# Kernel tuning notes

Hardware: AMD Instinct MI355X
Metric: run time of the kernel (lower is better)

The kernel has to match this reference:

```python
import jax, jax.numpy as jnp
import numpy as np

MG = (5, 5)          # mesh_grid_size
UP = (17, 17)        # upsample_size
IMG = (512.0, 512.0) # image_size
B = 8192
FC_OUT = MG[0] * MG[1] * 2  # 50
KH = (UP[0] - 1) // (MG[0] - 1) + 1  # 5
KW = (UP[1] - 1) // (MG[1] - 1) + 1  # 5
SH = (UP[0] - 1) // (MG[0] - 1)      # 4
SW = (UP[1] - 1) // (MG[1] - 1)      # 4
L0 = MG[0] - 1
L1 = MG[1] - 1


def _grid(h, w):
    # channel 0: x coords vary along rows (image_size[0]); channel 1: y along cols
    x_t = jnp.broadcast_to(jnp.linspace(0.0, IMG[0], h)[:, None], (h, w))
    y_t = jnp.broadcast_to(jnp.linspace(0.0, IMG[1], w)[None, :], (h, w))
    return jnp.stack([x_t, y_t], 0)  # [2, h, w]


def _unfold22(a):
    # a: [B, 2, H, W] -> [B, (H-1)*(W-1), 4, 2]; 4 = kernel positions row-major, 2 = channel
    p = jnp.stack([a[:, :, :-1, :-1], a[:, :, :-1, 1:],
                   a[:, :, 1:, :-1], a[:, :, 1:, 1:]], axis=2)  # [B,2,4,H-1,W-1]
    return p.reshape(a.shape[0], 2, 4, -1).transpose(0, 3, 2, 1)


def _persp(src, dst):
    # exact 4-point homography solve (torchgeometry.get_perspective_transform)
    x0, y0 = src[..., 0], src[..., 1]
    u, v = dst[..., 0], dst[..., 1]
    z = jnp.zeros_like(x0)
    o = jnp.ones_like(x0)
    ax = jnp.stack([x0, y0, o, z, z, z, -u * x0, -u * y0], -1)  # [N,4,8]
    ay = jnp.stack([z, z, z, x0, y0, o, -v * x0, -v * y0], -1)
    A = jnp.concatenate([ax, ay], 1)                 # [N,8,8]
    bb = jnp.concatenate([u, v], 1)[..., None]       # [N,8,1]
    h = jnp.linalg.solve(A, bb)[..., 0]              # [N,8]
    return jnp.concatenate([h, o[:, :1]], 1).reshape(-1, 3, 3)


def setup_inputs() -> dict:
    key = jax.random.key(0)
    ks = jax.random.split(key, 4)
    def lin(k, i, o):
        return jax.random.normal(k, (i, o), jnp.float32) / jnp.sqrt(i)
    return {
        "x": jax.random.normal(ks[0], (B, 1024), jnp.float32),
        "W1": lin(ks[1], 1024, 1024), "b1": jnp.zeros((1024,), jnp.float32),
        "W2": lin(ks[2], 1024, 2048), "b2": jnp.zeros((2048,), jnp.float32),
        "W3": lin(ks[3], 2048, FC_OUT), "b3": jnp.zeros((FC_OUT,), jnp.float32),
    }


def reference(x, W1, b1, W2, b2, W3, b3):
    Bn = x.shape[0]
    h = jax.nn.relu(x @ W1 + b1)
    h = jax.nn.relu(h @ W2 + b2)
    out = (h @ W3 + b3).reshape(Bn, 2, MG[0], MG[1])  # [B,2,5,5] mesh flow

    # sparse control grid and 2x2 patch corner points
    gs = _grid(MG[0], MG[1])
    src = _unfold22(jnp.broadcast_to(gs[None], (Bn, 2, MG[0], MG[1]))).reshape(-1, 4, 2)
    flow = _unfold22(out).reshape(-1, 4, 2)
    M = _persp(src, src + flow)  # [B*16, 3, 3]

    # dense grid and its unfold2 (kernel KHxKW, stride SHxSW) patch points
    gd = _grid(UP[0], UP[1])  # [2, 17, 17]
    gi = (np.arange(L0) * SH)[:, None, None, None] + np.arange(KH)[None, None, :, None]
    gj = (np.arange(L1) * SW)[None, :, None, None] + np.arange(KW)[None, None, None, :]
    I, J = np.broadcast_arrays(gi, gj)  # [L0,L1,KH,KW]
    pts = gd[:, I, J].transpose(1, 2, 3, 4, 0).reshape(1, L0 * L1, KH * KW, 2)
    pts = jnp.broadcast_to(pts, (Bn, L0 * L1, KH * KW, 2)).reshape(Bn * L0 * L1, KH * KW, 2)

    # transform_points: homogeneous warp + perspective divide
    ph = jnp.concatenate([pts, jnp.ones(pts.shape[:-1] + (1,), pts.dtype)], -1)
    oh = jnp.einsum('nij,npj->npi', M, ph)
    warped = oh[..., :2] / oh[..., 2:3]
    warped = warped.reshape(Bn, L0, L1, KH, KW, 2)

    # Fold: scatter-accumulate overlapping patches
    fold = jnp.zeros((Bn, 2, UP[0], UP[1]), x.dtype)
    for i in range(L0):
        for j in range(L1):
            blk = warped[:, i, j].transpose(0, 3, 1, 2)  # [B,2,KH,KW]
            fold = fold.at[:, :, i * SH:i * SH + KH, j * SW:j * SW + KW].add(blk)

    # boundary rescaling exactly as the torch code: only the 5x5 crossing points
    idx = np.arange(0, UP[0], MG[0] - 1)
    X, Y = np.meshgrid(idx, idx, indexing='xy')
    fold = fold.at[:, :, X, Y].multiply(0.5)
    for (a, b) in ((0, 0), (0, UP[1] - 1), (UP[0] - 1, UP[1] - 1), (UP[0] - 1, 0)):
        fold = fold.at[:, :, a, b].multiply(2.0)

    return fold - gd[None]  # upsampled mesh flow [B,2,17,17]
```

## Files before the change

kernel.cpp:

```cpp
#include <hip/hip_runtime.h>

typedef __bf16 bf16x8 __attribute__((ext_vector_type(8)));
typedef float f32x4 __attribute__((ext_vector_type(4)));

__device__ __forceinline__ unsigned short f2bf(float f) {
  unsigned int u = __builtin_bit_cast(unsigned int, f);
  unsigned int r = (u + 0x7fffu + ((u >> 16) & 1u)) >> 16;
  return (unsigned short)r;
}

__device__ __forceinline__ float bf2f(unsigned short u) {
  unsigned int v = ((unsigned int)u) << 16;
  return __builtin_bit_cast(float, v);
}

__device__ __forceinline__ void load16_lds(const unsigned short* g, unsigned short* l) {
  __builtin_amdgcn_global_load_lds(
      (const __attribute__((address_space(1))) void*)g,
      (__attribute__((address_space(3))) void*)l, 16, 0, 0);
}

__device__ __forceinline__ void wait_vm0() {
  asm volatile("s_waitcnt vmcnt(0)" ::: "memory");
  __builtin_amdgcn_sched_barrier(0);
}
__device__ __forceinline__ void barrier_raw() {
  __builtin_amdgcn_sched_barrier(0);
  __builtin_amdgcn_s_barrier();
  __builtin_amdgcn_sched_barrier(0);
}


__global__ __launch_bounds__(256) void prepass(
    const float* __restrict__ x, const float* __restrict__ W1,
    const float* __restrict__ W2, const float* __restrict__ W3,
    unsigned short* __restrict__ xbf, unsigned short* __restrict__ w1t,
    unsigned short* __restrict__ w2t, unsigned short* __restrict__ w3t) {
  __shared__ float tile[32][33];
  const int bid = blockIdx.x;
  const int t = threadIdx.x;
  if (bid < 2048) {
    for (int i = bid * 256 + t; i < 2097152; i += 2048 * 256) {
      float4 f = ((const float4*)x)[i];
      uint2 o;
      o.x = (unsigned)f2bf(f.x) | ((unsigned)f2bf(f.y) << 16);
      o.y = (unsigned)f2bf(f.z) | ((unsigned)f2bf(f.w) << 16);
      ((uint2*)xbf)[i] = o;
    }
  } else if (bid < 3072) {
    int ti = bid - 2048;
    int n0 = (ti & 31) * 32, k0 = (ti >> 5) * 32;
    int tx = t & 31, ty = t >> 5;
    #pragma unroll
    for (int r = 0; r < 32; r += 8)
      tile[ty + r][tx] = W1[(size_t)(k0 + ty + r) * 1024 + n0 + tx];
    __syncthreads();
    #pragma unroll
    for (int r = 0; r < 32; r += 8)
      w1t[(size_t)(n0 + ty + r) * 1024 + k0 + tx] = f2bf(tile[tx][ty + r]);
  } else if (bid < 5120) {
    int ti = bid - 3072;
    int n0 = (ti & 63) * 32, k0 = (ti >> 6) * 32;
    int tx = t & 31, ty = t >> 5;
    #pragma unroll
    for (int r = 0; r < 32; r += 8)
      tile[ty + r][tx] = W2[(size_t)(k0 + ty + r) * 2048 + n0 + tx];
    __syncthreads();
    #pragma unroll
    for (int r = 0; r < 32; r += 8)
      w2t[(size_t)(n0 + ty + r) * 1024 + k0 + tx] = f2bf(tile[tx][ty + r]);
  } else {
    int idx = (bid - 5120) * 256 + t;
    int n = idx >> 11, k = idx & 2047;
    w3t[idx] = f2bf((n < 50) ? W3[(size_t)k * 50 + n] : 0.f);
  }
}


__global__ __launch_bounds__(512, 4) void gemm1_v9(
    const unsigned short* __restrict__ A,
    const unsigned short* __restrict__ Bt,
    const float* __restrict__ bias,
    unsigned short* __restrict__ C) {
  constexpr int K = 1024, N = 1024, NT = 32;
  constexpr int AEL = 128 * 32;
  constexpr int BUF = 2 * AEL;
  __shared__ __align__(16) unsigned short smem[2 * BUF];
  const int t = threadIdx.x;
  const int m0 = blockIdx.x * 128;
  const int n0 = blockIdx.y * 128;
  const int lane = t & 63, wv = t >> 6;
  const int l16 = lane & 15, quad = lane >> 4;
  const int rb = (wv >> 1) * 32, cb = (wv & 1) * 64;

  const int tr = t >> 2;
  const int cg = ((t & 3) - (tr >> 1)) & 3;
  const unsigned short* Ag0 = A + (size_t)(m0 + tr) * K + cg * 8;
  const unsigned short* Bg0 = Bt + (size_t)(n0 + tr) * K + cg * 8;
  const int ldsO = wv * 512;

  f32x4 acc[2][4] = {};

  load16_lds(Ag0, &smem[ldsO]);
  load16_lds(Bg0, &smem[AEL + ldsO]);

  for (int kt = 0; kt < NT; ++kt) {
    unsigned short* Ls = &smem[(kt & 1) * BUF];

    wait_vm0();
    barrier_raw();

    if (kt + 1 < NT) {
      unsigned short* Ln = &smem[((kt + 1) & 1) * BUF];
      load16_lds(Ag0 + (size_t)(kt + 1) * 32, &Ln[ldsO]);
      load16_lds(Bg0 + (size_t)(kt + 1) * 32, &Ln[AEL + ldsO]);
    }

    bf16x8 af[2], bfr[4];
    #pragma unroll
    for (int ni = 0; ni < 4; ++ni) {
      int row = cb + ni * 16 + l16;
      bfr[ni] = *(const bf16x8*)&Ls[AEL + row * 32 + ((quad + (row >> 1)) & 3) * 8];
    }
    #pragma unroll
    for (int mi = 0; mi < 2; ++mi) {
      int row = rb + mi * 16 + l16;
      af[mi] = *(const bf16x8*)&Ls[row * 32 + ((quad + (row >> 1)) & 3) * 8];
    }
    #pragma unroll
    for (int mi = 0; mi < 2; ++mi)
      #pragma unroll
      for (int ni = 0; ni < 4; ++ni)
        acc[mi][ni] = __builtin_amdgcn_mfma_f32_16x16x32_bf16(
            af[mi], bfr[ni], acc[mi][ni], 0, 0, 0);
  }
  barrier_raw();

  unsigned short* Cs = smem;
  float bv[4];
  #pragma unroll
  for (int ni = 0; ni < 4; ++ni) bv[ni] = bias[n0 + cb + ni * 16 + l16];
  #pragma unroll
  for (int mi = 0; mi < 2; ++mi)
    #pragma unroll
    for (int ni = 0; ni < 4; ++ni)
      #pragma unroll
      for (int r = 0; r < 4; ++r) {
        int row = rb + mi * 16 + quad * 4 + r;
        int col = cb + ni * 16 + l16;
        int pb = (col >> 3) ^ (row & 15);
        Cs[row * 128 + pb * 8 + (col & 7)] = f2bf(fmaxf(acc[mi][ni][r] + bv[ni], 0.f));
      }
  __syncthreads();
  #pragma unroll
  for (int j = 0; j < 4; ++j) {
    int idx = j * 512 + t;
    int row = idx >> 4, cgc = idx & 15;
    int pb = cgc ^ (row & 15);
    *(uint4*)&C[(size_t)(m0 + row) * N + n0 + cgc * 8] =
        *(const uint4*)&Cs[row * 128 + pb * 8];
  }
}


__global__ __launch_bounds__(512, 4) void gemm2_v8(
    const unsigned short* __restrict__ A,
    const unsigned short* __restrict__ Bt,
    const float* __restrict__ bias,
    const unsigned short* __restrict__ W3t,
    unsigned short* __restrict__ part) {
  constexpr int K = 1024, NT = 32;
  constexpr int AEL = 256 * 32;
  constexpr int BEL = 128 * 32;
  constexpr int BUF = AEL + BEL;
  __shared__ __align__(16) unsigned short smem[32768];
  const int t = threadIdx.x;
  const int m0 = blockIdx.x * 256;
  const int n0 = blockIdx.y * 128;
  const int lane = t & 63, wv = t >> 6;
  const int l16 = lane & 15, quad = lane >> 4;
  const int rb = (wv >> 1) * 64, cb = (wv & 1) * 64;

  const int tr = t >> 2;
  const int cg = ((t & 3) - (tr >> 1)) & 3;
  const unsigned short* Ag0 = A + (size_t)(m0 + tr) * K + cg * 8;
  const unsigned short* Bg0 = Bt + (size_t)(n0 + tr) * K + cg * 8;
  const int ldsO = wv * 512;

  f32x4 acc[4][4] = {};

  load16_lds(Ag0, &smem[ldsO]);
  load16_lds(Ag0 + (size_t)128 * K, &smem[4096 + ldsO]);
  load16_lds(Bg0, &smem[AEL + ldsO]);

  for (int kt = 0; kt < NT; ++kt) {
    unsigned short* Ls = &smem[(kt & 1) * BUF];

    wait_vm0();
    barrier_raw();

    if (kt + 1 < NT) {
      unsigned short* Ln = &smem[((kt + 1) & 1) * BUF];
      const unsigned short* An = Ag0 + (size_t)(kt + 1) * 32;
      const unsigned short* Bn = Bg0 + (size_t)(kt + 1) * 32;
      load16_lds(An, &Ln[ldsO]);
      load16_lds(An + (size_t)128 * K, &Ln[4096 + ldsO]);
      load16_lds(Bn, &Ln[AEL + ldsO]);
    }

    bf16x8 af[4], bfr[4];
    #pragma unroll
    for (int ni = 0; ni < 4; ++ni) {
      int row = cb + ni * 16 + l16;
      bfr[ni] = *(const bf16x8*)&Ls[AEL + row * 32 + ((quad + (row >> 1)) & 3) * 8];
    }
    #pragma unroll
    for (int mi = 0; mi < 4; ++mi) {
      int row = rb + mi * 16 + l16;
      af[mi] = *(const bf16x8*)&Ls[row * 32 + ((quad + (row >> 1)) & 3) * 8];
    }
    #pragma unroll
    for (int mi = 0; mi < 4; ++mi)
      #pragma unroll
      for (int ni = 0; ni < 4; ++ni)
        acc[mi][ni] = __builtin_amdgcn_mfma_f32_16x16x32_bf16(
            af[mi], bfr[ni], acc[mi][ni], 0, 0, 0);
  }
  barrier_raw();

  unsigned short* Cs = smem;
  float bv[4];
  #pragma unroll
  for (int ni = 0; ni < 4; ++ni) bv[ni] = bias[n0 + cb + ni * 16 + l16];
  #pragma unroll
  for (int mi = 0; mi < 4; ++mi)
    #pragma unroll
    for (int ni = 0; ni < 4; ++ni)
      #pragma unroll
      for (int r = 0; r < 4; ++r) {
        int row = rb + mi * 16 + quad * 4 + r;
        int col = cb + ni * 16 + l16;
        int pb = (col >> 3) ^ (row & 15);
        Cs[row * 128 + pb * 8 + (col & 7)] = f2bf(fmaxf(acc[mi][ni][r] + bv[ni], 0.f));
      }
  __syncthreads();

  bf16x8 bq[4][4];
  #pragma unroll
  for (int ks = 0; ks < 4; ++ks)
    #pragma unroll
    for (int nt = 0; nt < 4; ++nt)
      bq[ks][nt] = *(const bf16x8*)&W3t[(size_t)(nt * 16 + l16) * 2048 +
                                        n0 + ks * 32 + quad * 8];
  f32x4 acc2[2][4] = {};
  #pragma unroll
  for (int ks = 0; ks < 4; ++ks) {
    bf16x8 af2[2];
    #pragma unroll
    for (int mt = 0; mt < 2; ++mt) {
      int row = wv * 32 + mt * 16 + l16;
      int pb = (ks * 4 + quad) ^ (row & 15);
      af2[mt] = *(const bf16x8*)&Cs[row * 128 + pb * 8];
    }
    #pragma unroll
    for (int mt = 0; mt < 2; ++mt)
      #pragma unroll
      for (int nt = 0; nt < 4; ++nt)
        acc2[mt][nt] = __builtin_amdgcn_mfma_f32_16x16x32_bf16(
            af2[mt], bq[ks][nt], acc2[mt][nt], 0, 0, 0);
  }

  const int zi = blockIdx.y;
  #pragma unroll
  for (int mt = 0; mt < 2; ++mt)
    #pragma unroll
    for (int nt = 0; nt < 4; ++nt) {
      int col = nt * 16 + l16;
      #pragma unroll
      for (int r = 0; r < 4; ++r) {
        int row = m0 + wv * 32 + mt * 16 + quad * 4 + r;
        part[((size_t)row * 16 + zi) * 64 + col] = f2bf(acc2[mt][nt][r]);
      }
    }
}


__global__ __launch_bounds__(256) void geom_reduce(
    const unsigned short* __restrict__ part,
    const float* __restrict__ b3,
    float* __restrict__ outp) {
  __shared__ float s_out3[16 * 64];
  __shared__ float unfold[16][16][50];
  const int t = threadIdx.x;
  const int bbase = blockIdx.x * 16;

  for (int i = t; i < 1024; i += 256) {
    int m = i >> 6, n = i & 63;
    const unsigned short* p = part + ((size_t)(bbase + m) * 16) * 64 + n;
    float v = 0.f;
    #pragma unroll
    for (int z = 0; z < 16; ++z) v += bf2f(p[z * 64]);
    s_out3[i] = v + ((n < 50) ? b3[n] : 0.f);
  }
  __syncthreads();

  {
    const int bl = t >> 4;
    const int p = t & 15;
    const int pi = p >> 2, pj = p & 3;
    const float* o = &s_out3[bl * 64];

    float u00 = 128.f * pi       + o[pi * 5 + pj];
    float v00 = 128.f * pj       + o[25 + pi * 5 + pj];
    float u01 = 128.f * pi       + o[pi * 5 + pj + 1];
    float v01 = 128.f * (pj + 1) + o[25 + pi * 5 + pj + 1];
    float u10 = 128.f * (pi + 1) + o[(pi + 1) * 5 + pj];
    float v10 = 128.f * pj       + o[25 + (pi + 1) * 5 + pj];
    float u11 = 128.f * (pi + 1) + o[(pi + 1) * 5 + pj + 1];
    float v11 = 128.f * (pj + 1) + o[25 + (pi + 1) * 5 + pj + 1];

    float sx = u00 - u10 + u11 - u01;
    float sy = v00 - v10 + v11 - v01;
    float dx1 = u10 - u11, dx2 = u01 - u11;
    float dy1 = v10 - v11, dy2 = v01 - v11;
    float rden = 1.f / (dx1 * dy2 - dx2 * dy1);
    float g = (sx * dy2 - dx2 * sy) * rden;
    float h = (dx1 * sy - sx * dy1) * rden;
    float a = u10 - u00 + g * u10;
    float b = u01 - u00 + h * u01;
    float c = u00;
    float d = v10 - v00 + g * v10;
    float e = v01 - v00 + h * v01;
    float f = v00;

    #pragma unroll
    for (int ai = 0; ai < 5; ++ai) {
      #pragma unroll
      for (int bi = 0; bi < 5; ++bi) {
        float s = 0.25f * ai, tt = 0.25f * bi;
        float rw = 1.f / (g * s + h * tt + 1.f);
        unfold[bl][p][ai * 5 + bi]      = (a * s + b * tt + c) * rw;
        unfold[bl][p][25 + ai * 5 + bi] = (d * s + e * tt + f) * rw;
      }
    }
  }
  __syncthreads();

  for (int i = t; i < 16 * 578; i += 256) {
    int blb = i / 578;
    int rem = i - blb * 578;
    int ch = rem / 289;
    int ij = rem - ch * 289;
    int gi = ij / 17, gj = ij - gi * 17;

    int pi0 = (gi == 16) ? 3 : (gi >> 2);
    int ai0 = gi - 4 * pi0;
    int ci = (((gi & 3) == 0) && gi != 0 && gi != 16) ? 2 : 1;
    int pj0 = (gj == 16) ? 3 : (gj >> 2);
    int bj0 = gj - 4 * pj0;
    int cj = (((gj & 3) == 0) && gj != 0 && gj != 16) ? 2 : 1;

    float val = 0.f;
    #pragma unroll
    for (int ii = 0; ii < 2; ++ii) {
      if (ii < ci) {
        int pi = pi0 - ii, ai = ii ? 4 : ai0;
        #pragma unroll
        for (int jj = 0; jj < 2; ++jj) {
          if (jj < cj) {
            int pj = pj0 - jj, bi = jj ? 4 : bj0;
            val += unfold[blb][pi * 4 + pj][ch * 25 + ai * 5 + bi];
          }
        }
      }
    }

    if (((gi & 3) == 0) && ((gj & 3) == 0)) val *= 0.5f;
    if ((gi == 0 || gi == 16) && (gj == 0 || gj == 16)) val *= 2.f;
    val -= (ch == 0) ? 32.f * gi : 32.f * gj;
    outp[(size_t)(bbase + blb) * 578 + rem] = val;
  }
}


extern "C" void kernel_launch(void* const* d_in, const int* in_sizes, int n_in,
                              void* d_out, int out_size, void* d_ws, size_t ws_size,
                              hipStream_t stream) {
  const float* x  = (const float*)d_in[0];
  const float* W1 = (const float*)d_in[1];
  const float* b1 = (const float*)d_in[2];
  const float* W2 = (const float*)d_in[3];
  const float* b2 = (const float*)d_in[4];
  const float* W3 = (const float*)d_in[5];
  const float* b3 = (const float*)d_in[6];
  float* outp = (float*)d_out;

  char* ws = (char*)d_ws;
  unsigned short* xbf = (unsigned short*)ws;
  unsigned short* w1t = (unsigned short*)(ws + (size_t)16 * 1024 * 1024);
  unsigned short* part = (unsigned short*)ws;
  unsigned short* w2t = (unsigned short*)(ws + (size_t)34 * 1024 * 1024);
  unsigned short* w3t = (unsigned short*)(ws + (size_t)38 * 1024 * 1024);
  unsigned short* h1  = (unsigned short*)(ws + (size_t)38 * 1024 * 1024 + 512 * 1024);

  prepass<<<5632, 256, 0, stream>>>(x, W1, W2, W3, xbf, w1t, w2t, w3t);

  gemm1_v9<<<dim3(64, 8), 512, 0, stream>>>(xbf, w1t, b1, h1);
  gemm2_v8<<<dim3(32, 16), 512, 0, stream>>>(h1, w2t, b2, w3t, part);
  geom_reduce<<<512, 256, 0, stream>>>(part, b3, outp);
}
```

Before: 181.5 us.

## Deepen GEMM LDS pipelines to four stages and enlarge GEMM2 tile to 256x256

Both GEMMs move from a two-buffer LDS scheme that waited for all loads to a four-slot ring with three K-tiles in flight, using partial vmcnt waits. The aim is to hide global-to-LDS latency behind MFMA work. GEMM2 also grows its output tile from 256x128 to 256x256, which halves the number of N-blocks and the partial sums written for the fused third layer. In exchange, occupancy bounds drop to 2 and 1 blocks per CU, register use rises, and only 256 blocks launch for GEMM2, which may underfill the device.

```diff
diff --git a/kernel.cpp b/kernel.cpp
--- a/kernel.cpp
+++ b/kernel.cpp
@@ -22,6 +22,18 @@
 
 __device__ __forceinline__ void wait_vm0() {
   asm volatile("s_waitcnt vmcnt(0)" ::: "memory");
+  __builtin_amdgcn_sched_barrier(0);
+}
+__device__ __forceinline__ void wait_vm2() {
+  asm volatile("s_waitcnt vmcnt(2)" ::: "memory");
+  __builtin_amdgcn_sched_barrier(0);
+}
+__device__ __forceinline__ void wait_vm4() {
+  asm volatile("s_waitcnt vmcnt(4)" ::: "memory");
+  __builtin_amdgcn_sched_barrier(0);
+}
+__device__ __forceinline__ void wait_vm8() {
+  asm volatile("s_waitcnt vmcnt(8)" ::: "memory");
   __builtin_amdgcn_sched_barrier(0);
 }
 __device__ __forceinline__ void barrier_raw() {
@@ -77,15 +89,14 @@
 }
 
 
-__global__ __launch_bounds__(512, 4) void gemm1_v9(
+__global__ __launch_bounds__(512, 2) void gemm1_v10(
     const unsigned short* __restrict__ A,
     const unsigned short* __restrict__ Bt,
     const float* __restrict__ bias,
     unsigned short* __restrict__ C) {
   constexpr int K = 1024, N = 1024, NT = 32;
-  constexpr int AEL = 128 * 32;
-  constexpr int BUF = 2 * AEL;
-  __shared__ __align__(16) unsigned short smem[2 * BUF];
+  constexpr int SLOT = 8192;
+  __shared__ __align__(16) unsigned short smem[4 * SLOT];
   const int t = threadIdx.x;
   const int m0 = blockIdx.x * 128;
   const int n0 = blockIdx.y * 128;
@@ -101,26 +112,31 @@
 
   f32x4 acc[2][4] = {};
 
-  load16_lds(Ag0, &smem[ldsO]);
-  load16_lds(Bg0, &smem[AEL + ldsO]);
+  #pragma unroll
+  for (int p = 0; p < 3; ++p) {
+    load16_lds(Ag0 + (size_t)p * 32, &smem[p * SLOT + ldsO]);
+    load16_lds(Bg0 + (size_t)p * 32, &smem[p * SLOT + 4096 + ldsO]);
+  }
 
   for (int kt = 0; kt < NT; ++kt) {
-    unsigned short* Ls = &smem[(kt & 1) * BUF];
-
-    wait_vm0();
+    unsigned short* Ls = &smem[(kt & 3) * SLOT];
+
+    if (kt < NT - 2) wait_vm4();
+    else if (kt == NT - 2) wait_vm2();
+    else wait_vm0();
     barrier_raw();
 
-    if (kt + 1 < NT) {
-      unsigned short* Ln = &smem[((kt + 1) & 1) * BUF];
-      load16_lds(Ag0 + (size_t)(kt + 1) * 32, &Ln[ldsO]);
-      load16_lds(Bg0 + (size_t)(kt + 1) * 32, &Ln[AEL + ldsO]);
+    if (kt + 3 < NT) {
+      unsigned short* Ln = &smem[((kt + 3) & 3) * SLOT];
+      load16_lds(Ag0 + (size_t)(kt + 3) * 32, &Ln[ldsO]);
+      load16_lds(Bg0 + (size_t)(kt + 3) * 32, &Ln[4096 + ldsO]);
     }
 
     bf16x8 af[2], bfr[4];
     #pragma unroll
     for (int ni = 0; ni < 4; ++ni) {
       int row = cb + ni * 16 + l16;
-      bfr[ni] = *(const bf16x8*)&Ls[AEL + row * 32 + ((quad + (row >> 1)) & 3) * 8];
+      bfr[ni] = *(const bf16x8*)&Ls[4096 + row * 32 + ((quad + (row >> 1)) & 3) * 8];
     }
     #pragma unroll
     for (int mi = 0; mi < 2; ++mi) {
@@ -163,23 +179,21 @@
 }
 
 
-__global__ __launch_bounds__(512, 4) void gemm2_v8(
+__global__ __launch_bounds__(512, 1) void gemm2_v10(
     const unsigned short* __restrict__ A,
     const unsigned short* __restrict__ Bt,
     const float* __restrict__ bias,
     const unsigned short* __restrict__ W3t,
     unsigned short* __restrict__ part) {
   constexpr int K = 1024, NT = 32;
-  constexpr int AEL = 256 * 32;
-  constexpr int BEL = 128 * 32;
-  constexpr int BUF = AEL + BEL;
-  __shared__ __align__(16) unsigned short smem[32768];
+  constexpr int SLOT = 16384;
+  __shared__ __align__(16) unsigned short smem[4 * SLOT];
   const int t = threadIdx.x;
   const int m0 = blockIdx.x * 256;
-  const int n0 = blockIdx.y * 128;
+  const int n0 = blockIdx.y * 256;
   const int lane = t & 63, wv = t >> 6;
   const int l16 = lane & 15, quad = lane >> 4;
-  const int rb = (wv >> 1) * 64, cb = (wv & 1) * 64;
+  const int rb = (wv >> 2) * 128, cb = (wv & 3) * 64;
 
   const int tr = t >> 2;
   const int cg = ((t & 3) - (tr >> 1)) & 3;
@@ -187,40 +201,48 @@
   const unsigned short* Bg0 = Bt + (size_t)(n0 + tr) * K + cg * 8;
   const int ldsO = wv * 512;
 
-  f32x4 acc[4][4] = {};
-
-  load16_lds(Ag0, &smem[ldsO]);
-  load16_lds(Ag0 + (size_t)128 * K, &smem[4096 + ldsO]);
-  load16_lds(Bg0, &smem[AEL + ldsO]);
+  f32x4 acc[8][4] = {};
+
+  #pragma unroll
+  for (int p = 0; p < 3; ++p) {
+    load16_lds(Ag0 + (size_t)p * 32, &smem[p * SLOT + ldsO]);
+    load16_lds(Ag0 + (size_t)128 * K + (size_t)p * 32, &smem[p * SLOT + 4096 + ldsO]);
+    load16_lds(Bg0 + (size_t)p * 32, &smem[p * SLOT + 8192 + ldsO]);
+    load16_lds(Bg0 + (size_t)128 * K + (size_t)p * 32, &smem[p * SLOT + 12288 + ldsO]);
+  }
 
   for (int kt = 0; kt < NT; ++kt) {
-    unsigned short* Ls = &smem[(kt & 1) * BUF];
-
-    wait_vm0();
+    unsigned short* Ls = &smem[(kt & 3) * SLOT];
+
+    if (kt < NT - 2) wait_vm8();
+    else if (kt == NT - 2) wait_vm4();
+    else wait_vm0();
     barrier_raw();
 
-    if (kt + 1 < NT) {
-      unsigned short* Ln = &smem[((kt + 1) & 1) * BUF];
-      const unsigned short* An = Ag0 + (size_t)(kt + 1) * 32;
-      const unsigned short* Bn = Bg0 + (size_t)(kt + 1) * 32;
+    if (kt + 3 < NT) {
+      unsigned short* Ln = &smem[((kt + 3) & 3) * SLOT];
+      const unsigned short* An = Ag0 + (size_t)(kt + 3) * 32;
+      const unsigned short* Bn = Bg0 + (size_t)(kt + 3) * 32;
       load16_lds(An, &Ln[ldsO]);
       load16_lds(An + (size_t)128 * K, &Ln[4096 + ldsO]);
-      load16_lds(Bn, &Ln[AEL + ldsO]);
-    }
-
-    bf16x8 af[4], bfr[4];
+      load16_lds(Bn, &Ln[8192 + ldsO]);
+      load16_lds(Bn + (size_t)128 * K, &Ln[12288 + ldsO]);
+    }
+
+    bf16x8 bfr[4];
     #pragma unroll
     for (int ni = 0; ni < 4; ++ni) {
       int row = cb + ni * 16 + l16;
-      bfr[ni] = *(const bf16x8*)&Ls[AEL + row * 32 + ((quad + (row >> 1)) & 3) * 8];
-    }
-    #pragma unroll
-    for (int mi = 0; mi < 4; ++mi) {
+      bfr[ni] = *(const bf16x8*)&Ls[8192 + row * 32 + ((quad + (row >> 1)) & 3) * 8];
+    }
+    bf16x8 af[8];
+    #pragma unroll
+    for (int mi = 0; mi < 8; ++mi) {
       int row = rb + mi * 16 + l16;
       af[mi] = *(const bf16x8*)&Ls[row * 32 + ((quad + (row >> 1)) & 3) * 8];
     }
     #pragma unroll
-    for (int mi = 0; mi < 4; ++mi)
+    for (int mi = 0; mi < 8; ++mi)
       #pragma unroll
       for (int ni = 0; ni < 4; ++ni)
         acc[mi][ni] = __builtin_amdgcn_mfma_f32_16x16x32_bf16(
@@ -233,34 +255,34 @@
   #pragma unroll
   for (int ni = 0; ni < 4; ++ni) bv[ni] = bias[n0 + cb + ni * 16 + l16];
   #pragma unroll
-  for (int mi = 0; mi < 4; ++mi)
+  for (int mi = 0; mi < 8; ++mi)
     #pragma unroll
     for (int ni = 0; ni < 4; ++ni)
       #pragma unroll
       for (int r = 0; r < 4; ++r) {
         int row = rb + mi * 16 + quad * 4 + r;
         int col = cb + ni * 16 + l16;
-        int pb = (col >> 3) ^ (row & 15);
-        Cs[row * 128 + pb * 8 + (col & 7)] = f2bf(fmaxf(acc[mi][ni][r] + bv[ni], 0.f));
+        int pb = (col >> 3) ^ (row & 31);
+        Cs[row * 256 + pb * 8 + (col & 7)] = f2bf(fmaxf(acc[mi][ni][r] + bv[ni], 0.f));
       }
   __syncthreads();
 
-  bf16x8 bq[4][4];
-  #pragma unroll
-  for (int ks = 0; ks < 4; ++ks)
+  bf16x8 bq[8][4];
+  #pragma unroll
+  for (int ks = 0; ks < 8; ++ks)
     #pragma unroll
     for (int nt = 0; nt < 4; ++nt)
       bq[ks][nt] = *(const bf16x8*)&W3t[(size_t)(nt * 16 + l16) * 2048 +
                                         n0 + ks * 32 + quad * 8];
   f32x4 acc2[2][4] = {};
   #pragma unroll
-  for (int ks = 0; ks < 4; ++ks) {
+  for (int ks = 0; ks < 8; ++ks) {
     bf16x8 af2[2];
     #pragma unroll
     for (int mt = 0; mt < 2; ++mt) {
       int row = wv * 32 + mt * 16 + l16;
-      int pb = (ks * 4 + quad) ^ (row & 15);
-      af2[mt] = *(const bf16x8*)&Cs[row * 128 + pb * 8];
+      int pb = (ks * 4 + quad) ^ (row & 31);
+      af2[mt] = *(const bf16x8*)&Cs[row * 256 + pb * 8];
     }
     #pragma unroll
     for (int mt = 0; mt < 2; ++mt)
@@ -279,7 +301,7 @@
       #pragma unroll
       for (int r = 0; r < 4; ++r) {
         int row = m0 + wv * 32 + mt * 16 + quad * 4 + r;
-        part[((size_t)row * 16 + zi) * 64 + col] = f2bf(acc2[mt][nt][r]);
+        part[((size_t)row * 8 + zi) * 64 + col] = f2bf(acc2[mt][nt][r]);
       }
     }
 }
@@ -296,10 +318,10 @@
 
   for (int i = t; i < 1024; i += 256) {
     int m = i >> 6, n = i & 63;
-    const unsigned short* p = part + ((size_t)(bbase + m) * 16) * 64 + n;
+    const unsigned short* p = part + ((size_t)(bbase + m) * 8) * 64 + n;
     float v = 0.f;
     #pragma unroll
-    for (int z = 0; z < 16; ++z) v += bf2f(p[z * 64]);
+    for (int z = 0; z < 8; ++z) v += bf2f(p[z * 64]);
     s_out3[i] = v + ((n < 50) ? b3[n] : 0.f);
   }
   __syncthreads();
@@ -405,7 +427,7 @@
 
   prepass<<<5632, 256, 0, stream>>>(x, W1, W2, W3, xbf, w1t, w2t, w3t);
 
-  gemm1_v9<<<dim3(64, 8), 512, 0, stream>>>(xbf, w1t, b1, h1);
-  gemm2_v8<<<dim3(32, 16), 512, 0, stream>>>(h1, w2t, b2, w3t, part);
+  gemm1_v10<<<dim3(64, 8), 512, 0, stream>>>(xbf, w1t, b1, h1);
+  gemm2_v10<<<dim3(32, 8), 512, 0, stream>>>(h1, w2t, b2, w3t, part);
   geom_reduce<<<512, 256, 0, stream>>>(part, b3, outp);
 }
```

Measured after the change: 183.4 us. About the same (+1.0%).
